# Optimization experiments

Measured on AMD Instinct MI355X. Metric: run time of the kernel, lower is better.

The kernel has to match this reference:

```python
import jax, jax.numpy as jnp
from jax import lax
import numpy as np

N_FEATURE = 128
EDGE = 12          # int(sqrt(128) + 1)
BATCH = 131072


def maxpool2(x):
    # 2x2 max pool, stride 2, NCHW
    return lax.reduce_window(x, -jnp.inf, lax.max,
                             (1, 1, 2, 2), (1, 1, 2, 2), 'VALID')


def conv3x3(x, w, b):
    # 3x3 conv, padding=1, NCHW / OIHW
    y = lax.conv_general_dilated(x, w, window_strides=(1, 1),
                                 padding=((1, 1), (1, 1)),
                                 dimension_numbers=('NCHW', 'OIHW', 'NCHW'))
    return y + b[None, :, None, None]


def setup_inputs() -> dict:
    key = jax.random.key(0)
    ks = jax.random.split(key, 9)
    x = jax.random.normal(ks[0], (BATCH, N_FEATURE), dtype=jnp.float32)
    conv1_w = jax.random.normal(ks[1], (3, 1, 3, 3), dtype=jnp.float32) * 0.1
    conv1_b = jnp.zeros((3,), dtype=jnp.float32)
    conv2_w = jax.random.normal(ks[2], (6, 3, 3, 3), dtype=jnp.float32) * 0.1
    conv2_b = jnp.zeros((6,), dtype=jnp.float32)
    fc1_w = jax.random.normal(ks[3], (128, 54), dtype=jnp.float32) * 0.1
    fc1_b = jnp.zeros((128,), dtype=jnp.float32)
    out_w = jax.random.normal(ks[4], (N_FEATURE, 128), dtype=jnp.float32) * 0.1
    out_b = jnp.zeros((N_FEATURE,), dtype=jnp.float32)
    return {"x": x, "conv1_w": conv1_w, "conv1_b": conv1_b,
            "conv2_w": conv2_w, "conv2_b": conv2_b,
            "fc1_w": fc1_w, "fc1_b": fc1_b,
            "out_w": out_w, "out_b": out_b}


def reference(x, conv1_w, conv1_b, conv2_w, conv2_b, fc1_w, fc1_b, out_w, out_b):
    num = x.shape[0]
    n = x.shape[1]                       # 128
    pad = EDGE * EDGE - n                # 16 trailing zeros
    # vectorized transto3D: row-major fill of edge x edge grid, zero-padded tail
    g = jnp.pad(x, ((0, 0), (0, pad))).reshape(num, 1, EDGE, EDGE)
    h = jax.nn.relu(maxpool2(conv3x3(g, conv1_w, conv1_b)))      # [num,3,6,6]
    h = jax.nn.relu(maxpool2(conv3x3(h, conv2_w, conv2_b)))      # [num,6,3,3]
    h = h.reshape(num, 54)
    h = jax.nn.relu(h @ fc1_w.T + fc1_b)                         # [num,128]
    return h @ out_w.T + out_b                                   # [num,128]
```

## Files before the change

kernel.cpp:

```cpp
#include <hip/hip_runtime.h>

typedef unsigned int uint;
typedef unsigned short ushort;

using bf16x8 = __attribute__((ext_vector_type(8))) short;
using f32x4  = __attribute__((ext_vector_type(4))) float;

__device__ __forceinline__ ushort f2b(float f) {
  union { float f; uint i; } v; v.f = f;
  uint r = (v.i + 0x7fffu + ((v.i >> 16) & 1u)) >> 16;
  return (ushort)r;
}
__device__ __forceinline__ bf16x8 ldfrag(const ushort* p) {
  union { uint4 u; bf16x8 v; } x; x.u = *(const uint4*)p; return x.v;
}

__global__ __launch_bounds__(256) void prep_kernel(
    const float* __restrict__ fc1w, const float* __restrict__ outw,
    ushort* __restrict__ ws) {
  const int t = threadIdx.x;
#pragma unroll
  for (int i = 0; i < 32; ++i) {
    const int idx = t * 32 + i;
    const int row = idx >> 6, k = idx & 63;
    ws[idx] = (k < 54) ? f2b(fc1w[row * 54 + k]) : (ushort)0;
  }
#pragma unroll
  for (int i = 0; i < 64; ++i) {
    const int idx = t * 64 + i;
    ws[8192 + idx] = f2b(outw[idx]);
  }
}

__global__ __launch_bounds__(256, 2) void fused_kernel(
    const float* __restrict__ x,
    const float* __restrict__ w1g, const float* __restrict__ b1g,
    const float* __restrict__ w2g, const float* __restrict__ b2g,
    const ushort* __restrict__ wsw,
    const float* __restrict__ fc1b, const float* __restrict__ outb,
    float* __restrict__ out) {
  __shared__ __align__(16) ushort h2A[256][72];
  __shared__ __align__(16) ushort tA[128][136];
  __shared__ float fb1[128], ob[128];

  const int t = threadIdx.x;
  const int s0 = blockIdx.x * 256;

  if (t < 128) { fb1[t] = fc1b[t]; ob[t] = outb[t]; }

  {
    const float* xs = x + (size_t)(s0 + t) * 128;
    float xv[128];
#pragma unroll
    for (int i = 0; i < 32; ++i) {
      const float4 v = ((const float4*)xs)[i];
      xv[4 * i + 0] = v.x; xv[4 * i + 1] = v.y;
      xv[4 * i + 2] = v.z; xv[4 * i + 3] = v.w;
    }

    float w1[3][9], b1[3];
#pragma unroll
    for (int c = 0; c < 3; ++c) {
      b1[c] = b1g[c];
#pragma unroll
      for (int q = 0; q < 9; ++q) w1[c][q] = w1g[c * 9 + q];
    }

    float h1[3][6][6];
#pragma unroll
    for (int pr = 0; pr < 6; ++pr)
#pragma unroll
      for (int pc = 0; pc < 6; ++pc)
#pragma unroll
        for (int ch = 0; ch < 3; ++ch) {
          float m = -3.0e38f;
#pragma unroll
          for (int dr = 0; dr < 2; ++dr)
#pragma unroll
            for (int dc = 0; dc < 2; ++dc) {
              float a = 0.f;
#pragma unroll
              for (int ky = 0; ky < 3; ++ky)
#pragma unroll
                for (int kx = 0; kx < 3; ++kx) {
                  const int r = 2 * pr + dr + ky - 1;
                  const int c = 2 * pc + dc + kx - 1;
                  if (r >= 0 && r < 12 && c >= 0 && c < 12 && (12 * r + c) < 128)
                    a = fmaf(w1[ch][ky * 3 + kx], xv[12 * r + c], a);
                }
              m = fmaxf(m, a);
            }
          h1[ch][pr][pc] = fmaxf(m + b1[ch], 0.f);
        }

    float h2[54];
#pragma unroll
    for (int o = 0; o < 6; ++o) {
      float w2[27];
#pragma unroll
      for (int q = 0; q < 27; ++q) w2[q] = w2g[o * 27 + q];
      const float bo = b2g[o];
#pragma unroll
      for (int qr = 0; qr < 3; ++qr)
#pragma unroll
        for (int qc = 0; qc < 3; ++qc) {
          float m = -3.0e38f;
#pragma unroll
          for (int dr = 0; dr < 2; ++dr)
#pragma unroll
            for (int dc = 0; dc < 2; ++dc) {
              float a = 0.f;
#pragma unroll
              for (int i = 0; i < 3; ++i)
#pragma unroll
                for (int ky = 0; ky < 3; ++ky)
#pragma unroll
                  for (int kx = 0; kx < 3; ++kx) {
                    const int yy = 2 * qr + dr + ky - 1;
                    const int xx = 2 * qc + dc + kx - 1;
                    if (yy >= 0 && yy < 6 && xx >= 0 && xx < 6)
                      a = fmaf(w2[i * 9 + ky * 3 + kx], h1[i][yy][xx], a);
                  }
              m = fmaxf(m, a);
            }
          h2[o * 9 + qr * 3 + qc] = fmaxf(m + bo, 0.f);
        }
    }

    uint pk[32];
#pragma unroll
    for (int q = 0; q < 27; ++q)
      pk[q] = (uint)f2b(h2[2 * q]) | ((uint)f2b(h2[2 * q + 1]) << 16);
#pragma unroll
    for (int q = 27; q < 32; ++q) pk[q] = 0u;
#pragma unroll
    for (int i = 0; i < 8; ++i) {
      uint4 v; v.x = pk[4 * i]; v.y = pk[4 * i + 1];
      v.z = pk[4 * i + 2]; v.w = pk[4 * i + 3];
      *(uint4*)&h2A[t][8 * i] = v;
    }
  }
  __syncthreads();

  const int lane = t & 63, wv = t >> 6;
  const int quad = lane >> 4, lm = lane & 15;
  const ushort* wsA = wsw;
  const ushort* wsB = wsw + 8192;

  for (int h = 0; h < 2; ++h) {
    f32x4 acc[2][8];
#pragma unroll
    for (int mt = 0; mt < 2; ++mt)
#pragma unroll
      for (int nt = 0; nt < 8; ++nt) acc[mt][nt] = (f32x4){0.f, 0.f, 0.f, 0.f};

#pragma unroll
    for (int kk = 0; kk < 2; ++kk) {
      const int ko = kk * 32 + quad * 8;
      bf16x8 a[2], b[8];
#pragma unroll
      for (int mt = 0; mt < 2; ++mt)
        a[mt] = ldfrag(&h2A[128 * h + 32 * wv + 16 * mt + lm][ko]);
#pragma unroll
      for (int nt = 0; nt < 8; ++nt)
        b[nt] = ldfrag(wsA + (16 * nt + lm) * 64 + ko);
#pragma unroll
      for (int mt = 0; mt < 2; ++mt)
#pragma unroll
        for (int nt = 0; nt < 8; ++nt)
          acc[mt][nt] = __builtin_amdgcn_mfma_f32_16x16x32_bf16(
              a[mt], b[nt], acc[mt][nt], 0, 0, 0);
    }

#pragma unroll
    for (int mt = 0; mt < 2; ++mt)
#pragma unroll
      for (int nt = 0; nt < 8; ++nt) {
        const int col = 16 * nt + lm;
        const float bj = fb1[col];
#pragma unroll
        for (int r = 0; r < 4; ++r) {
          const int row = 32 * wv + 16 * mt + quad * 4 + r;
          tA[row][col] = f2b(fmaxf(acc[mt][nt][r] + bj, 0.f));
        }
      }
    __syncthreads();

    f32x4 acc2[2][8];
#pragma unroll
    for (int mt = 0; mt < 2; ++mt)
#pragma unroll
      for (int nt = 0; nt < 8; ++nt) acc2[mt][nt] = (f32x4){0.f, 0.f, 0.f, 0.f};

#pragma unroll
    for (int kk = 0; kk < 4; ++kk) {
      const int ko = kk * 32 + quad * 8;
      bf16x8 a[2], b[8];
#pragma unroll
      for (int mt = 0; mt < 2; ++mt)
        a[mt] = ldfrag(&tA[32 * wv + 16 * mt + lm][ko]);
#pragma unroll
      for (int nt = 0; nt < 8; ++nt)
        b[nt] = ldfrag(wsB + (16 * nt + lm) * 128 + ko);
#pragma unroll
      for (int mt = 0; mt < 2; ++mt)
#pragma unroll
        for (int nt = 0; nt < 8; ++nt)
          acc2[mt][nt] = __builtin_amdgcn_mfma_f32_16x16x32_bf16(
              a[mt], b[nt], acc2[mt][nt], 0, 0, 0);
    }

#pragma unroll
    for (int mt = 0; mt < 2; ++mt)
#pragma unroll
      for (int nt = 0; nt < 8; ++nt) {
        const int col = 16 * nt + lm;
        const float bo = ob[col];
#pragma unroll
        for (int r = 0; r < 4; ++r) {
          const int srow = s0 + 128 * h + 32 * wv + 16 * mt + quad * 4 + r;
          out[(size_t)srow * 128 + col] = acc2[mt][nt][r] + bo;
        }
      }
    __syncthreads();
  }
}

extern "C" void kernel_launch(void* const* d_in, const int* in_sizes, int n_in,
                              void* d_out, int out_size, void* d_ws, size_t ws_size,
                              hipStream_t stream) {
  const float* x    = (const float*)d_in[0];
  const float* w1   = (const float*)d_in[1];
  const float* b1   = (const float*)d_in[2];
  const float* w2   = (const float*)d_in[3];
  const float* b2   = (const float*)d_in[4];
  const float* fc1w = (const float*)d_in[5];
  const float* fc1b = (const float*)d_in[6];
  const float* outw = (const float*)d_in[7];
  const float* outb = (const float*)d_in[8];
  float* outp = (float*)d_out;
  ushort* ws  = (ushort*)d_ws;

  const int N = in_sizes[0] / 128;

  prep_kernel<<<1, 256, 0, stream>>>(fc1w, outw, ws);
  fused_kernel<<<N / 256, 256, 0, stream>>>(x, w1, b1, w2, b2, ws,
                                            fc1b, outb, outp);
}
```

Baseline: 171.4 us.

## Shrink MLP tiles per wave, raise occupancy, and parallelize weight prep

```diff
diff --git a/kernel.cpp b/kernel.cpp
--- a/kernel.cpp
+++ b/kernel.cpp
@@ -18,21 +18,17 @@
 __global__ __launch_bounds__(256) void prep_kernel(
     const float* __restrict__ fc1w, const float* __restrict__ outw,
     ushort* __restrict__ ws) {
-  const int t = threadIdx.x;
-#pragma unroll
-  for (int i = 0; i < 32; ++i) {
-    const int idx = t * 32 + i;
-    const int row = idx >> 6, k = idx & 63;
-    ws[idx] = (k < 54) ? f2b(fc1w[row * 54 + k]) : (ushort)0;
-  }
-#pragma unroll
-  for (int i = 0; i < 64; ++i) {
-    const int idx = t * 64 + i;
-    ws[8192 + idx] = f2b(outw[idx]);
-  }
-}
-
-__global__ __launch_bounds__(256, 2) void fused_kernel(
+  const int g = blockIdx.x * 256 + threadIdx.x;
+  if (g < 8192) {
+    const int row = g >> 6, k = g & 63;
+    ws[g] = (k < 54) ? f2b(fc1w[row * 54 + k]) : (ushort)0;
+  } else {
+    const int idx = g - 8192;
+    ws[g] = f2b(outw[idx]);
+  }
+}
+
+__global__ __launch_bounds__(256, 3) void fused_kernel(
     const float* __restrict__ x,
     const float* __restrict__ w1g, const float* __restrict__ b1g,
     const float* __restrict__ w2g, const float* __restrict__ b2g,
@@ -40,13 +36,12 @@
     const float* __restrict__ fc1b, const float* __restrict__ outb,
     float* __restrict__ out) {
   __shared__ __align__(16) ushort h2A[256][72];
-  __shared__ __align__(16) ushort tA[128][136];
-  __shared__ float fb1[128], ob[128];
+  __shared__ __align__(16) ushort tA[64][136];
 
   const int t = threadIdx.x;
   const int s0 = blockIdx.x * 256;
-
-  if (t < 128) { fb1[t] = fc1b[t]; ob[t] = outb[t]; }
+  const int lane = t & 63, wv = t >> 6;
+  const int quad = lane >> 4, lm = lane & 15;
 
   {
     const float* xs = x + (size_t)(s0 + t) * 128;
@@ -140,88 +135,73 @@
       *(uint4*)&h2A[t][8 * i] = v;
     }
   }
+
+  float fb1r[8], obr[8];
+#pragma unroll
+  for (int nt = 0; nt < 8; ++nt) {
+    fb1r[nt] = fc1b[16 * nt + lm];
+    obr[nt]  = outb[16 * nt + lm];
+  }
   __syncthreads();
 
-  const int lane = t & 63, wv = t >> 6;
-  const int quad = lane >> 4, lm = lane & 15;
   const ushort* wsA = wsw;
   const ushort* wsB = wsw + 8192;
 
-  for (int h = 0; h < 2; ++h) {
-    f32x4 acc[2][8];
-#pragma unroll
-    for (int mt = 0; mt < 2; ++mt)
-#pragma unroll
-      for (int nt = 0; nt < 8; ++nt) acc[mt][nt] = (f32x4){0.f, 0.f, 0.f, 0.f};
+  for (int h = 0; h < 4; ++h) {
+    f32x4 acc[8];
+#pragma unroll
+    for (int nt = 0; nt < 8; ++nt) acc[nt] = (f32x4){0.f, 0.f, 0.f, 0.f};
 
 #pragma unroll
     for (int kk = 0; kk < 2; ++kk) {
       const int ko = kk * 32 + quad * 8;
-      bf16x8 a[2], b[8];
-#pragma unroll
-      for (int mt = 0; mt < 2; ++mt)
-        a[mt] = ldfrag(&h2A[128 * h + 32 * wv + 16 * mt + lm][ko]);
+      const bf16x8 a = ldfrag(&h2A[64 * h + 16 * wv + lm][ko]);
+      bf16x8 b[8];
 #pragma unroll
       for (int nt = 0; nt < 8; ++nt)
         b[nt] = ldfrag(wsA + (16 * nt + lm) * 64 + ko);
 #pragma unroll
-      for (int mt = 0; mt < 2; ++mt)
-#pragma unroll
-        for (int nt = 0; nt < 8; ++nt)
-          acc[mt][nt] = __builtin_amdgcn_mfma_f32_16x16x32_bf16(
-              a[mt], b[nt], acc[mt][nt], 0, 0, 0);
-    }
-
-#pragma unroll
-    for (int mt = 0; mt < 2; ++mt)
-#pragma unroll
-      for (int nt = 0; nt < 8; ++nt) {
-        const int col = 16 * nt + lm;
-        const float bj = fb1[col];
-#pragma unroll
-        for (int r = 0; r < 4; ++r) {
-          const int row = 32 * wv + 16 * mt + quad * 4 + r;
-          tA[row][col] = f2b(fmaxf(acc[mt][nt][r] + bj, 0.f));
-        }
-      }
+      for (int nt = 0; nt < 8; ++nt)
+        acc[nt] = __builtin_amdgcn_mfma_f32_16x16x32_bf16(a, b[nt], acc[nt],
+                                                          0, 0, 0);
+    }
+
+#pragma unroll
+    for (int nt = 0; nt < 8; ++nt) {
+      const int col = 16 * nt + lm;
+#pragma unroll
+      for (int r = 0; r < 4; ++r)
+        tA[16 * wv + quad * 4 + r][col] = f2b(fmaxf(acc[nt][r] + fb1r[nt], 0.f));
+    }
     __syncthreads();
 
-    f32x4 acc2[2][8];
-#pragma unroll
-    for (int mt = 0; mt < 2; ++mt)
-#pragma unroll
-      for (int nt = 0; nt < 8; ++nt) acc2[mt][nt] = (f32x4){0.f, 0.f, 0.f, 0.f};
+    f32x4 acc2[8];
+#pragma unroll
+    for (int nt = 0; nt < 8; ++nt) acc2[nt] = (f32x4){0.f, 0.f, 0.f, 0.f};
 
 #pragma unroll
     for (int kk = 0; kk < 4; ++kk) {
       const int ko = kk * 32 + quad * 8;
-      bf16x8 a[2], b[8];
-#pragma unroll
-      for (int mt = 0; mt < 2; ++mt)
-        a[mt] = ldfrag(&tA[32 * wv + 16 * mt + lm][ko]);
+      const bf16x8 a = ldfrag(&tA[16 * wv + lm][ko]);
+      bf16x8 b[8];
 #pragma unroll
       for (int nt = 0; nt < 8; ++nt)
         b[nt] = ldfrag(wsB + (16 * nt + lm) * 128 + ko);
 #pragma unroll
-      for (int mt = 0; mt < 2; ++mt)
-#pragma unroll
-        for (int nt = 0; nt < 8; ++nt)
-          acc2[mt][nt] = __builtin_amdgcn_mfma_f32_16x16x32_bf16(
-              a[mt], b[nt], acc2[mt][nt], 0, 0, 0);
-    }
-
-#pragma unroll
-    for (int mt = 0; mt < 2; ++mt)
-#pragma unroll
-      for (int nt = 0; nt < 8; ++nt) {
-        const int col = 16 * nt + lm;
-        const float bo = ob[col];
-#pragma unroll
-        for (int r = 0; r < 4; ++r) {
-          const int srow = s0 + 128 * h + 32 * wv + 16 * mt + quad * 4 + r;
-          out[(size_t)srow * 128 + col] = acc2[mt][nt][r] + bo;
-        }
+      for (int nt = 0; nt < 8; ++nt)
+        acc2[nt] = __builtin_amdgcn_mfma_f32_16x16x32_bf16(a, b[nt], acc2[nt],
+                                                           0, 0, 0);
+    }
+
+#pragma unroll
+    for (int nt = 0; nt < 8; ++nt) {
+      const int col = 16 * nt + lm;
+#pragma unroll
+      for (int r = 0; r < 4; ++r) {
+        const int srow = s0 + 64 * h + 16 * wv + quad * 4 + r;
+        out[(size_t)srow * 128 + col] = acc2[nt][r] + obr[nt];
       }
+    }
     __syncthreads();
   }
 }
@@ -243,7 +223,7 @@
 
   const int N = in_sizes[0] / 128;
 
-  prep_kernel<<<1, 256, 0, stream>>>(fc1w, outw, ws);
+  prep_kernel<<<96, 256, 0, stream>>>(fc1w, outw, ws);
   fused_kernel<<<N / 256, 256, 0, stream>>>(x, w1, b1, w2, b2, ws,
                                             fc1b, outb, outp);
 }
```

Result: slower. 186.4 us (+8.7%).
